# Kernel tuning notes

Measured on AMD Instinct MI355X. Metric: run time of the kernel, lower is better.

Reference implementation:

```python
import jax, jax.numpy as jnp
import numpy as np

EPS = 1e-06


def setup_inputs() -> dict:
    key = jax.random.key(0)
    k1, k2 = jax.random.split(key)
    B, C, H, W = 16, 4, 1024, 1024
    prd = jax.random.uniform(k1, (B, C, H, W), dtype=jnp.float32)
    tgt = jax.random.uniform(k2, (B, C, H, W), dtype=jnp.float32)
    return {"prd": prd, "tgt": tgt}


def reference(prd, tgt):
    # Per-(b, c) reductions over spatial dims, all fused into batched ops.
    inter = jnp.einsum("bchw,bchw->bc", prd, tgt)                 # dot(prd, tgt)
    union = jnp.sum(prd, axis=(2, 3)) + jnp.sum(tgt, axis=(2, 3)) + EPS
    dice_bc = (2.0 * inter + EPS) / union                          # (B, C)
    # _dice_coeff averages over batch; reduction='none' -> per-channel scores (C,)
    return jnp.mean(dice_bc, axis=0)
```

## Files before the change

kernel.cpp:

```cpp
#include <hip/hip_runtime.h>


#define HW   (1024 * 1024)
#define NB   16
#define NC   4
#define NBC  (NB * NC)
#define BPS  64
#define TPB  256
#define EPSF 1e-6f

__global__ void zero_ws_kernel(float* __restrict__ ws) {
    int i = threadIdx.x;
    if (i < NBC * 3) ws[i] = 0.0f;
}

__global__ __launch_bounds__(TPB) void dice_partial_kernel(
        const float* __restrict__ prd,
        const float* __restrict__ tgt,
        float* __restrict__ ws) {
    const int bc = blockIdx.y;
    const float4* __restrict__ p4 = (const float4*)(prd + (size_t)bc * HW);
    const float4* __restrict__ t4 = (const float4*)(tgt + (size_t)bc * HW);
    const int n4 = HW / 4;

    float inter = 0.0f, sp = 0.0f, st = 0.0f;
    for (int i = blockIdx.x * TPB + threadIdx.x; i < n4; i += BPS * TPB) {
        float4 a = p4[i];
        float4 b = t4[i];
        inter += a.x * b.x + a.y * b.y + a.z * b.z + a.w * b.w;
        sp    += a.x + a.y + a.z + a.w;
        st    += b.x + b.y + b.z + b.w;
    }

    #pragma unroll
    for (int off = 32; off > 0; off >>= 1) {
        inter += __shfl_down(inter, off);
        sp    += __shfl_down(sp, off);
        st    += __shfl_down(st, off);
    }

    __shared__ float s[3][TPB / 64];
    const int wave = threadIdx.x >> 6;
    const int lane = threadIdx.x & 63;
    if (lane == 0) {
        s[0][wave] = inter;
        s[1][wave] = sp;
        s[2][wave] = st;
    }
    __syncthreads();
    if (threadIdx.x == 0) {
        float ti = s[0][0] + s[0][1] + s[0][2] + s[0][3];
        float tp = s[1][0] + s[1][1] + s[1][2] + s[1][3];
        float tt = s[2][0] + s[2][1] + s[2][2] + s[2][3];
        atomicAdd(&ws[bc * 3 + 0], ti);
        atomicAdd(&ws[bc * 3 + 1], tp);
        atomicAdd(&ws[bc * 3 + 2], tt);
    }
}

__global__ void dice_final_kernel(const float* __restrict__ ws,
                                  float* __restrict__ out) {
    __shared__ float dice[NBC];
    const int bc = threadIdx.x;
    if (bc < NBC) {
        float inter = ws[bc * 3 + 0];
        float uni   = ws[bc * 3 + 1] + ws[bc * 3 + 2] + EPSF;
        dice[bc] = (2.0f * inter + EPSF) / uni;
    }
    __syncthreads();
    if (bc < NC) {
        float s = 0.0f;
        #pragma unroll
        for (int b = 0; b < NB; ++b) s += dice[b * NC + bc];
        out[bc] = s / (float)NB;
    }
}

extern "C" void kernel_launch(void* const* d_in, const int* in_sizes, int n_in,
                              void* d_out, int out_size, void* d_ws, size_t ws_size,
                              hipStream_t stream) {
    const float* prd = (const float*)d_in[0];
    const float* tgt = (const float*)d_in[1];
    float* out = (float*)d_out;
    float* ws  = (float*)d_ws;

    zero_ws_kernel<<<1, 256, 0, stream>>>(ws);
    dice_partial_kernel<<<dim3(BPS, NBC), TPB, 0, stream>>>(prd, tgt, ws);
    dice_final_kernel<<<1, 64, 0, stream>>>(ws, out);
}
```

Measured before the change: 529.2 us.

## Unroll vector loads with nontemporal hints and replace atomics with per-block partials

The streaming loop is fully unrolled so each thread issues eight independent 16-byte nontemporal loads per step, raising memory-level parallelism. Per-block partial sums are written to distinct workspace slots and reduced in the final kernel, removing atomics and the separate zeroing kernel launch. This needs a larger workspace and hard-codes an exact trip count for the fixed problem size.

New measurement: 473.8 us. 1.12x faster.

```diff
diff --git a/kernel.cpp b/kernel.cpp
--- a/kernel.cpp
+++ b/kernel.cpp
@@ -7,29 +7,44 @@
 #define NBC  (NB * NC)
 #define BPS  64
 #define TPB  256
+#define NBLK (NBC * BPS)
 #define EPSF 1e-6f
 
-__global__ void zero_ws_kernel(float* __restrict__ ws) {
-    int i = threadIdx.x;
-    if (i < NBC * 3) ws[i] = 0.0f;
-}
+typedef float vf4 __attribute__((ext_vector_type(4)));
 
 __global__ __launch_bounds__(TPB) void dice_partial_kernel(
         const float* __restrict__ prd,
         const float* __restrict__ tgt,
         float* __restrict__ ws) {
     const int bc = blockIdx.y;
-    const float4* __restrict__ p4 = (const float4*)(prd + (size_t)bc * HW);
-    const float4* __restrict__ t4 = (const float4*)(tgt + (size_t)bc * HW);
-    const int n4 = HW / 4;
+    const vf4* __restrict__ p4 = (const vf4*)(prd + (size_t)bc * HW);
+    const vf4* __restrict__ t4 = (const vf4*)(tgt + (size_t)bc * HW);
+
+    const int S   = BPS * TPB;
+    const int tid = blockIdx.x * TPB + threadIdx.x;
 
     float inter = 0.0f, sp = 0.0f, st = 0.0f;
-    for (int i = blockIdx.x * TPB + threadIdx.x; i < n4; i += BPS * TPB) {
-        float4 a = p4[i];
-        float4 b = t4[i];
-        inter += a.x * b.x + a.y * b.y + a.z * b.z + a.w * b.w;
-        sp    += a.x + a.y + a.z + a.w;
-        st    += b.x + b.y + b.z + b.w;
+
+    #pragma unroll
+    for (int g = 0; g < 4; ++g) {
+        const int i = tid + g * 4 * S;
+        vf4 a0 = __builtin_nontemporal_load(p4 + i);
+        vf4 a1 = __builtin_nontemporal_load(p4 + i + S);
+        vf4 a2 = __builtin_nontemporal_load(p4 + i + 2 * S);
+        vf4 a3 = __builtin_nontemporal_load(p4 + i + 3 * S);
+        vf4 b0 = __builtin_nontemporal_load(t4 + i);
+        vf4 b1 = __builtin_nontemporal_load(t4 + i + S);
+        vf4 b2 = __builtin_nontemporal_load(t4 + i + 2 * S);
+        vf4 b3 = __builtin_nontemporal_load(t4 + i + 3 * S);
+
+        inter += a0.x * b0.x + a0.y * b0.y + a0.z * b0.z + a0.w * b0.w;
+        inter += a1.x * b1.x + a1.y * b1.y + a1.z * b1.z + a1.w * b1.w;
+        inter += a2.x * b2.x + a2.y * b2.y + a2.z * b2.z + a2.w * b2.w;
+        inter += a3.x * b3.x + a3.y * b3.y + a3.z * b3.z + a3.w * b3.w;
+        sp += (a0.x + a0.y + a0.z + a0.w) + (a1.x + a1.y + a1.z + a1.w)
+            + (a2.x + a2.y + a2.z + a2.w) + (a3.x + a3.y + a3.z + a3.w);
+        st += (b0.x + b0.y + b0.z + b0.w) + (b1.x + b1.y + b1.z + b1.w)
+            + (b2.x + b2.y + b2.z + b2.w) + (b3.x + b3.y + b3.z + b3.w);
     }
 
     #pragma unroll
@@ -49,12 +64,10 @@
     }
     __syncthreads();
     if (threadIdx.x == 0) {
-        float ti = s[0][0] + s[0][1] + s[0][2] + s[0][3];
-        float tp = s[1][0] + s[1][1] + s[1][2] + s[1][3];
-        float tt = s[2][0] + s[2][1] + s[2][2] + s[2][3];
-        atomicAdd(&ws[bc * 3 + 0], ti);
-        atomicAdd(&ws[bc * 3 + 1], tp);
-        atomicAdd(&ws[bc * 3 + 2], tt);
+        const int slot = bc * BPS + blockIdx.x;
+        ws[0 * NBLK + slot] = s[0][0] + s[0][1] + s[0][2] + s[0][3];
+        ws[1 * NBLK + slot] = s[1][0] + s[1][1] + s[1][2] + s[1][3];
+        ws[2 * NBLK + slot] = s[2][0] + s[2][1] + s[2][2] + s[2][3];
     }
 }
 
@@ -63,9 +76,15 @@
     __shared__ float dice[NBC];
     const int bc = threadIdx.x;
     if (bc < NBC) {
-        float inter = ws[bc * 3 + 0];
-        float uni   = ws[bc * 3 + 1] + ws[bc * 3 + 2] + EPSF;
-        dice[bc] = (2.0f * inter + EPSF) / uni;
+        float inter = 0.0f, sp = 0.0f, st = 0.0f;
+        #pragma unroll 8
+        for (int k = 0; k < BPS; ++k) {
+            const int slot = bc * BPS + k;
+            inter += ws[0 * NBLK + slot];
+            sp    += ws[1 * NBLK + slot];
+            st    += ws[2 * NBLK + slot];
+        }
+        dice[bc] = (2.0f * inter + EPSF) / (sp + st + EPSF);
     }
     __syncthreads();
     if (bc < NC) {
@@ -84,7 +103,6 @@
     float* out = (float*)d_out;
     float* ws  = (float*)d_ws;
 
-    zero_ws_kernel<<<1, 256, 0, stream>>>(ws);
     dice_partial_kernel<<<dim3(BPS, NBC), TPB, 0, stream>>>(prd, tgt, ws);
     dice_final_kernel<<<1, 64, 0, stream>>>(ws, out);
 }
```
